# Performance work log

Hardware: AMD Instinct MI355X
Metric: run time of the kernel (lower is better)

Reference implementation:

```python
import math
import jax, jax.numpy as jnp
import numpy as np

T, B, C, H = 1024, 4, 1024, 16
D = C // H  # d_k = 64


def setup_inputs() -> dict:
    key = jax.random.key(0)
    ks = jax.random.split(key, 16)
    s = 0.02
    return {
        "query": jax.random.normal(ks[0], (T, B, C), jnp.float32),
        "key": jax.random.normal(ks[1], (T, B, C), jnp.float32),
        "value": jax.random.normal(ks[2], (T, B, C), jnp.float32),
        "pos_emb": jax.random.normal(ks[3], (2 * T - 1, 1, C), jnp.float32),
        "Wq": jax.random.normal(ks[4], (C, C), jnp.float32) * s,
        "bq": jnp.zeros((C,), jnp.float32),
        "Wk": jax.random.normal(ks[5], (C, C), jnp.float32) * s,
        "bk": jnp.zeros((C,), jnp.float32),
        "Wv": jax.random.normal(ks[6], (C, C), jnp.float32) * s,
        "bv": jnp.zeros((C,), jnp.float32),
        "Wp": jax.random.normal(ks[7], (C, C), jnp.float32) * s,
        "Wo": jax.random.normal(ks[8], (C, C), jnp.float32) * s,
        "bo": jnp.zeros((C,), jnp.float32),
        "pos_bias_u": jax.random.normal(ks[9], (H, D), jnp.float32) * s,
        "pos_bias_v": jax.random.normal(ks[10], (H, D), jnp.float32) * s,
    }


def rel_shift(x):
    # x: [B, H, T, P] with P = 2T-1 -> [B, H, T, T]
    b, h, t, p = x.shape
    x = jnp.pad(x, ((0, 0), (0, 0), (0, 0), (1, 0)))  # [B,H,T,P+1]
    x = x.reshape(b, h, p + 1, t)[:, :, 1:, :].reshape(b, h, t, p)
    return x[..., : p // 2 + 1]


def reference(query, key, value, pos_emb, Wq, bq, Wk, bk, Wv, bv, Wp, Wo, bo,
              pos_bias_u, pos_bias_v):
    # T x B x C -> B x T x C
    q_in = query.transpose(1, 0, 2)
    k_in = key.transpose(1, 0, 2)
    v_in = value.transpose(1, 0, 2)
    p_in = pos_emb.transpose(1, 0, 2)  # [1, 2T-1, C]

    q = (q_in @ Wq.T + bq).reshape(B, T, H, D)            # [B,T,H,D]
    k = (k_in @ Wk.T + bk).reshape(B, T, H, D)
    v = (v_in @ Wv.T + bv).reshape(B, T, H, D)
    p = (p_in @ Wp.T).reshape(2 * T - 1, H, D)            # [2T-1,H,D]

    # content (ac) and position (bd) scores
    matrix_ac = jnp.einsum('bthd,bshd->bhts', q + pos_bias_u, k)   # [B,H,T,T]
    matrix_bd = jnp.einsum('bthd,phd->bhtp', q + pos_bias_v, p)    # [B,H,T,2T-1]
    matrix_bd = rel_shift(matrix_bd)                               # [B,H,T,T]

    scores = (matrix_ac + matrix_bd) / math.sqrt(D)
    scores = jnp.clip(scores, -1e8, 1e8)
    attn = jax.nn.softmax(scores.astype(jnp.float32), axis=-1).astype(scores.dtype)

    x = jnp.einsum('bhts,bshd->bthd', attn, v).reshape(B, T, C)
    out = x @ Wo.T + bo
    return out.transpose(1, 0, 2)  # T x B x C
```

## Files before the change

kernel.cpp:

```cpp
#include <hip/hip_runtime.h>
#include <hip/hip_bf16.h>
#include <math.h>

#define T_SEQ 1024
#define NB 4
#define NH 16
#define DD 64
#define CC 1024

typedef __attribute__((ext_vector_type(8))) short short8;
typedef __attribute__((ext_vector_type(4))) float floatx4;
typedef __attribute__((ext_vector_type(4))) unsigned short ushort4v;

#define MFMA(a, b, c) __builtin_amdgcn_mfma_f32_16x16x32_bf16((a), (b), (c), 0, 0, 0)

__device__ inline float bf2f(unsigned short u) {
  union { unsigned int i; float f; } c; c.i = ((unsigned int)u) << 16; return c.f;
}
__device__ inline unsigned short f2bf(float x) {
  union { float f; unsigned int i; } c; c.f = x;
  unsigned int u = c.i;
  u += 0x7fff + ((u >> 16) & 1);
  return (unsigned short)(u >> 16);
}

__device__ __forceinline__ void gload_lds16(const void* g, void* l) {
  __builtin_amdgcn_global_load_lds(
      (const __attribute__((address_space(1))) unsigned int*)g,
      (__attribute__((address_space(3))) unsigned int*)l, 16, 0, 0);
}

__global__ __launch_bounds__(256) void convert_kernel(
    const float* __restrict__ q, const float* __restrict__ k,
    const float* __restrict__ v, const float* __restrict__ pe_in,
    const float* __restrict__ wq, const float* __restrict__ wk,
    const float* __restrict__ wv, const float* __restrict__ wp,
    const float* __restrict__ wo,
    unsigned short* __restrict__ qo, unsigned short* __restrict__ ko,
    unsigned short* __restrict__ vo, unsigned short* __restrict__ po,
    unsigned short* __restrict__ wqo, unsigned short* __restrict__ wko,
    unsigned short* __restrict__ wvo, unsigned short* __restrict__ wpo,
    unsigned short* __restrict__ woo)
{
  const int i = blockIdx.x * 256 + threadIdx.x;
  const float* src; unsigned short* dst; int off;
  if      (i < 524288)  { src = q;     dst = qo;  off = i; }
  else if (i < 1048576) { src = k;     dst = ko;  off = i - 524288; }
  else if (i < 1572864) { src = v;     dst = vo;  off = i - 1048576; }
  else if (i < 1834880) { src = pe_in; dst = po;  off = i - 1572864; }
  else if (i < 1965952) { src = wq;    dst = wqo; off = i - 1834880; }
  else if (i < 2097024) { src = wk;    dst = wko; off = i - 1965952; }
  else if (i < 2228096) { src = wv;    dst = wvo; off = i - 2097024; }
  else if (i < 2359168) { src = wp;    dst = wpo; off = i - 2228096; }
  else if (i < 2490240) { src = wo;    dst = woo; off = i - 2359168; }
  else {
    const int j = i - 2490240;
    *(short8*)&po[2047 * 1024 + j * 8] = (short8){0, 0, 0, 0, 0, 0, 0, 0};
    return;
  }
  const float4 a0 = *(const float4*)(src + (size_t)off * 8);
  const float4 a1 = *(const float4*)(src + (size_t)off * 8 + 4);
  short8 val = (short8){(short)f2bf(a0.x), (short)f2bf(a0.y), (short)f2bf(a0.z), (short)f2bf(a0.w),
                        (short)f2bf(a1.x), (short)f2bf(a1.y), (short)f2bf(a1.z), (short)f2bf(a1.w)};
  *(short8*)&dst[(size_t)off * 8] = val;
}

template <int OUT_BF16>
__device__ __forceinline__ void gemm_core(
    const unsigned short* __restrict__ A, const unsigned short* __restrict__ Wt,
    const float* __restrict__ bias, void* __restrict__ Cv,
    unsigned short* As, unsigned short* Bs, int N, int K, int bm, int bn)
{
  const int tid = threadIdx.x;
  const int lane = tid & 63;
  const int w = tid >> 6;
  const int l15 = lane & 15, quad = lane >> 4;
  const int rw = (w >> 1) * 64, cw = (w & 1) * 64;

  floatx4 acc[4][4];
#pragma unroll
  for (int i = 0; i < 4; ++i)
#pragma unroll
    for (int j = 0; j < 4; ++j) acc[i][j] = (floatx4){0.f, 0.f, 0.f, 0.f};

  const int lrow = lane >> 2, lcol = (lane & 3) * 8;
  const unsigned short* Ag = A + (size_t)(bm + w * 32 + lrow) * K + lcol;
  const unsigned short* Wg = Wt + (size_t)(bn + w * 32 + lrow) * K + lcol;
  unsigned short* AsW = As + w * 1024;
  unsigned short* BsW = Bs + w * 1024;

  for (int k0 = 0; k0 < K; k0 += 32) {
    gload_lds16(Ag + k0, AsW);
    gload_lds16(Ag + 16 * K + k0, AsW + 512);
    gload_lds16(Wg + k0, BsW);
    gload_lds16(Wg + 16 * K + k0, BsW + 512);
    __syncthreads();

    short8 af[4], bfr[4];
#pragma unroll
    for (int i = 0; i < 4; ++i)
      af[i] = *(short8*)&As[(rw + i * 16 + l15) * 32 + quad * 8];
#pragma unroll
    for (int j = 0; j < 4; ++j)
      bfr[j] = *(short8*)&Bs[(cw + j * 16 + l15) * 32 + quad * 8];
#pragma unroll
    for (int i = 0; i < 4; ++i)
#pragma unroll
      for (int j = 0; j < 4; ++j)
        acc[i][j] = MFMA(af[i], bfr[j], acc[i][j]);
    __syncthreads();
  }

#pragma unroll
  for (int j = 0; j < 4; ++j) {
    const int col = bn + cw + j * 16 + l15;
    const float bj = bias ? bias[col] : 0.f;
#pragma unroll
    for (int i = 0; i < 4; ++i) {
      const int row0 = bm + rw + i * 16 + quad * 4;
#pragma unroll
      for (int reg = 0; reg < 4; ++reg) {
        const float v = acc[i][j][reg] + bj;
        if (OUT_BF16)
          ((unsigned short*)Cv)[(size_t)(row0 + reg) * N + col] = f2bf(v);
        else
          ((float*)Cv)[(size_t)(row0 + reg) * N + col] = v;
      }
    }
  }
}

struct GemmJob { const unsigned short* A; const unsigned short* Wt;
                 const float* bias; unsigned short* C; int mtiles; };
struct GemmJobs { GemmJob j[4]; };

__global__ __launch_bounds__(256) void gemm_qkvp(GemmJobs jobs) {
  __shared__ __align__(16) unsigned short As[128 * 32];
  __shared__ __align__(16) unsigned short Bs[128 * 32];
  GemmJob jb = jobs.j[blockIdx.z];
  if ((int)blockIdx.y >= jb.mtiles) return;
  gemm_core<1>(jb.A, jb.Wt, jb.bias, jb.C, As, Bs, 1024, 1024,
               blockIdx.y * 128, blockIdx.x * 128);
}

template <int OUT_BF16>
__global__ __launch_bounds__(256) void gemm_one(
    const unsigned short* __restrict__ A, const unsigned short* __restrict__ Wt,
    const float* __restrict__ bias, void* __restrict__ Cv) {
  __shared__ __align__(16) unsigned short As[128 * 32];
  __shared__ __align__(16) unsigned short Bs[128 * 32];
  gemm_core<OUT_BF16>(A, Wt, bias, Cv, As, Bs, 1024, 1024,
                      blockIdx.y * 128, blockIdx.x * 128);
}

__global__ __launch_bounds__(256) void transpose_v(
    const unsigned short* __restrict__ vb, unsigned short* __restrict__ vT)
{
  __shared__ __align__(16) unsigned short Lt[64 * 136];
  const int t0 = blockIdx.x * 128;
  const int h = blockIdx.y, b = blockIdx.z;
  const int tid = threadIdx.x;

#pragma unroll
  for (int cc = 0; cc < 4; ++cc) {
    const int idx = tid + cc * 256;
    const int r = idx >> 3, pc = idx & 7;
    short8 val = *(const short8*)(vb + ((size_t)((t0 + r) * 4 + b)) * 1024 + h * 64 + pc * 8);
#pragma unroll
    for (int e = 0; e < 8; ++e)
      Lt[(pc * 8 + e) * 136 + r] = (unsigned short)val[e];
  }
  __syncthreads();
#pragma unroll
  for (int cc = 0; cc < 4; ++cc) {
    const int idx = tid + cc * 256;
    const int d = idx >> 4, tc = idx & 15;
    short8 v2 = *(short8*)&Lt[d * 136 + tc * 8];
    *(short8*)(vT + ((size_t)((b * 16 + h) * 64 + d)) * 1024 + t0 + tc * 8) = v2;
  }
}

__global__ __launch_bounds__(256) void precompute_kernel(
    const unsigned short* __restrict__ kb, const unsigned short* __restrict__ pb,
    const float* __restrict__ pbu, const float* __restrict__ pbv,
    float* __restrict__ uk, float* __restrict__ vp)
{
  const int i = blockIdx.x * 256 + threadIdx.x;
  if (i < 65536) {
    const int b = i >> 14, h = (i >> 10) & 15, s = i & 1023;
    const unsigned short* kr = kb + ((size_t)(s * 4 + b)) * 1024 + h * 64;
    const float* ur = pbu + h * 64;
    float sum = 0.f;
#pragma unroll
    for (int c = 0; c < 8; ++c) {
      short8 kv = *(const short8*)(kr + c * 8);
#pragma unroll
      for (int e = 0; e < 8; ++e) sum += bf2f((unsigned short)kv[e]) * ur[c * 8 + e];
    }
    uk[i] = sum;
  } else if (i < 98304) {
    const int j = i - 65536;
    const int idx = j >> 4, h = j & 15;
    const unsigned short* pr = pb + (size_t)idx * 1024 + h * 64;
    const float* vr = pbv + h * 64;
    float sum = 0.f;
#pragma unroll
    for (int c = 0; c < 8; ++c) {
      short8 pv = *(const short8*)(pr + c * 8);
#pragma unroll
      for (int e = 0; e < 8; ++e) sum += bf2f((unsigned short)pv[e]) * vr[c * 8 + e];
    }
    vp[(idx << 4) + h] = sum;
  }
}

__global__ __launch_bounds__(256) void attn_kernel(
    const unsigned short* __restrict__ qb, const unsigned short* __restrict__ kb,
    const unsigned short* __restrict__ pb, const unsigned short* __restrict__ vT,
    const float* __restrict__ uk, const float* __restrict__ vp,
    unsigned short* __restrict__ xb)
{
  __shared__ __align__(16) unsigned char SU[64 * 196 * 4];
  float* BDf = (float*)SU;
  unsigned short* Pb = (unsigned short*)SU;
  __shared__ float uk_s[128], vp_w[192];
  __shared__ float pmax[2][64], psum[2][64];
  __shared__ float alpha_s[64];

  const int tid = threadIdx.x;
  const int lane = tid & 63;
  const int w = tid >> 6;
  const int l15 = lane & 15, quad = lane >> 4;
  const int th = w & 1, sh = w >> 1;

  const int flat = blockIdx.x + (blockIdx.y << 4) + (blockIdx.z << 8);
  const int x8 = flat & 7, s8 = flat >> 3;
  const int hb = x8 * 8 + (s8 >> 4);
  const int t0 = (s8 & 15) * 64;
  const int b = hb >> 4, h = hb & 15;

  short8 qf[2][2];
#pragma unroll
  for (int tt = 0; tt < 2; ++tt)
#pragma unroll
    for (int kk = 0; kk < 2; ++kk) {
      const int t = t0 + th * 32 + tt * 16 + l15;
      qf[tt][kk] = *(const short8*)(qb + ((size_t)(t * 4 + b)) * 1024 + h * 64 + kk * 32 + quad * 8);
    }

  floatx4 of[2][2];
#pragma unroll
  for (int i = 0; i < 2; ++i)
#pragma unroll
    for (int j = 0; j < 2; ++j) of[i][j] = (floatx4){0.f, 0.f, 0.f, 0.f};

  float m_reg[2] = {-3.0e38f, -3.0e38f};
  float l_reg[2][4] = {{0.f, 0.f, 0.f, 0.f}, {0.f, 0.f, 0.f, 0.f}};

  for (int s0 = 0; s0 < 1024; s0 += 128) {
    const int w0 = s0 - t0 + 960;

    if (tid < 128) uk_s[tid] = uk[((b * 16 + h) << 10) + s0 + tid];
    if (tid < 192) vp_w[tid] = vp[(((size_t)(w0 + tid)) << 4) + h];

#pragma unroll
    for (int jt = 0; jt < 6; ++jt) {
      const int jj = sh * 96 + jt * 16 + l15;
      const unsigned short* pr = pb + ((size_t)(w0 + jj)) * 1024 + h * 64;
      short8 pf0 = *(const short8*)(pr + quad * 8);
      short8 pf1 = *(const short8*)(pr + 32 + quad * 8);
#pragma unroll
      for (int tt = 0; tt < 2; ++tt) {
        floatx4 z = (floatx4){0.f, 0.f, 0.f, 0.f};
        z = MFMA(pf0, qf[tt][0], z);
        z = MFMA(pf1, qf[tt][1], z);
        const int tloc = th * 32 + tt * 16 + l15;
        const int jjb = sh * 96 + jt * 16 + quad * 4;
        *(float4*)&BDf[tloc * 196 + jjb] = make_float4(z[0], z[1], z[2], z[3]);
      }
    }

    floatx4 st[4][2];
#pragma unroll
    for (int stile = 0; stile < 4; ++stile) {
      const int srow = s0 + sh * 64 + stile * 16 + l15;
      const unsigned short* kr = kb + ((size_t)(srow * 4 + b)) * 1024 + h * 64;
      short8 kf0 = *(const short8*)(kr + quad * 8);
      short8 kf1 = *(const short8*)(kr + 32 + quad * 8);
#pragma unroll
      for (int tt = 0; tt < 2; ++tt) {
        floatx4 z = (floatx4){0.f, 0.f, 0.f, 0.f};
        z = MFMA(kf0, qf[tt][0], z);
        z = MFMA(kf1, qf[tt][1], z);
        st[stile][tt] = z;
      }
    }
    __syncthreads();

    float lmax[2] = {-3.0e38f, -3.0e38f};
#pragma unroll
    for (int stile = 0; stile < 4; ++stile)
#pragma unroll
      for (int tt = 0; tt < 2; ++tt) {
        const int tloc = th * 32 + tt * 16 + l15;
#pragma unroll
        for (int reg = 0; reg < 4; ++reg) {
          const int sloc = sh * 64 + stile * 16 + quad * 4 + reg;
          const int jj = sloc - tloc + 63;
          float v = 0.125f * (st[stile][tt][reg] + BDf[tloc * 196 + jj] +
                              uk_s[sloc] + vp_w[jj]);
          st[stile][tt][reg] = v;
          lmax[tt] = fmaxf(lmax[tt], v);
        }
      }
#pragma unroll
    for (int tt = 0; tt < 2; ++tt) {
      lmax[tt] = fmaxf(lmax[tt], __shfl_xor(lmax[tt], 16));
      lmax[tt] = fmaxf(lmax[tt], __shfl_xor(lmax[tt], 32));
    }
    if (quad == 0) {
      pmax[sh][th * 32 + l15] = lmax[0];
      pmax[sh][th * 32 + 16 + l15] = lmax[1];
    }
    __syncthreads();

    float alpha_sc[2];
#pragma unroll
    for (int tt = 0; tt < 2; ++tt) {
      const int t = th * 32 + tt * 16 + l15;
      const float mn = fmaxf(m_reg[tt], fmaxf(pmax[0][t], pmax[1][t]));
      alpha_sc[tt] = __expf(m_reg[tt] - mn);
      m_reg[tt] = mn;
    }
    if (sh == 0 && quad == 0) {
      alpha_s[th * 32 + l15] = alpha_sc[0];
      alpha_s[th * 32 + 16 + l15] = alpha_sc[1];
    }
    float lsum[2] = {0.f, 0.f};
#pragma unroll
    for (int stile = 0; stile < 4; ++stile)
#pragma unroll
      for (int tt = 0; tt < 2; ++tt) {
        float p0 = __expf(st[stile][tt][0] - m_reg[tt]);
        float p1 = __expf(st[stile][tt][1] - m_reg[tt]);
        float p2 = __expf(st[stile][tt][2] - m_reg[tt]);
        float p3 = __expf(st[stile][tt][3] - m_reg[tt]);
        lsum[tt] += p0 + p1 + p2 + p3;
        const int tloc = th * 32 + tt * 16 + l15;
        const int sb = sh * 64 + stile * 16 + quad * 4;
        ushort4v pk = (ushort4v){f2bf(p0), f2bf(p1), f2bf(p2), f2bf(p3)};
        *(ushort4v*)&Pb[tloc * 136 + sb] = pk;
      }
#pragma unroll
    for (int tt = 0; tt < 2; ++tt) {
      lsum[tt] += __shfl_xor(lsum[tt], 16);
      lsum[tt] += __shfl_xor(lsum[tt], 32);
    }
    if (quad == 0) {
      psum[sh][th * 32 + l15] = lsum[0];
      psum[sh][th * 32 + 16 + l15] = lsum[1];
    }
    __syncthreads();

#pragma unroll
    for (int tt = 0; tt < 2; ++tt)
#pragma unroll
      for (int reg = 0; reg < 4; ++reg) {
        const int t = th * 32 + tt * 16 + quad * 4 + reg;
        const float ar = alpha_s[t];
        of[tt][0][reg] *= ar;
        of[tt][1][reg] *= ar;
        l_reg[tt][reg] = l_reg[tt][reg] * ar + psum[0][t] + psum[1][t];
      }
#pragma unroll
    for (int kk2 = 0; kk2 < 4; ++kk2) {
      short8 pa[2], vf[2];
#pragma unroll
      for (int tt = 0; tt < 2; ++tt)
        pa[tt] = *(short8*)&Pb[(th * 32 + tt * 16 + l15) * 136 + kk2 * 32 + quad * 8];
#pragma unroll
      for (int dt = 0; dt < 2; ++dt)
        vf[dt] = *(const short8*)(vT + ((size_t)((b * 16 + h) * 64 + sh * 32 + dt * 16 + l15)) * 1024 +
                                  s0 + kk2 * 32 + quad * 8);
#pragma unroll
      for (int tt = 0; tt < 2; ++tt)
#pragma unroll
        for (int dt = 0; dt < 2; ++dt)
          of[tt][dt] = MFMA(pa[tt], vf[kk2 * 0 + dt], of[tt][dt]);
    }
    __syncthreads();
  }

#pragma unroll
  for (int tt = 0; tt < 2; ++tt)
#pragma unroll
    for (int reg = 0; reg < 4; ++reg) {
      const int t = th * 32 + tt * 16 + quad * 4 + reg;
      const float il = 1.f / l_reg[tt][reg];
#pragma unroll
      for (int dt = 0; dt < 2; ++dt) {
        const int d = sh * 32 + dt * 16 + l15;
        xb[((size_t)((t0 + t) * 4 + b)) * 1024 + h * 64 + d] = f2bf(of[tt][dt][reg] * il);
      }
    }
}

extern "C" void kernel_launch(void* const* d_in, const int* in_sizes, int n_in,
                              void* d_out, int out_size, void* d_ws, size_t ws_size,
                              hipStream_t stream) {
  const float* query   = (const float*)d_in[0];
  const float* key_    = (const float*)d_in[1];
  const float* value   = (const float*)d_in[2];
  const float* pos_emb = (const float*)d_in[3];
  const float* Wq  = (const float*)d_in[4];
  const float* bq  = (const float*)d_in[5];
  const float* Wk  = (const float*)d_in[6];
  const float* bk  = (const float*)d_in[7];
  const float* Wv  = (const float*)d_in[8];
  const float* bv  = (const float*)d_in[9];
  const float* Wp  = (const float*)d_in[10];
  const float* Wo  = (const float*)d_in[11];
  const float* bo  = (const float*)d_in[12];
  const float* pbu = (const float*)d_in[13];
  const float* pbv = (const float*)d_in[14];
  float* out = (float*)d_out;

  unsigned short* U = (unsigned short*)d_ws;
  unsigned short* qin = U;
  unsigned short* kin = U + 4194304;
  unsigned short* vin = U + 8388608;
  unsigned short* pe  = U + 12582912;
  unsigned short* wq  = U + 14680064;
  unsigned short* wk  = U + 15728640;
  unsigned short* wv  = U + 16777216;
  unsigned short* wp  = U + 17825792;
  unsigned short* wo  = U + 18874368;
  unsigned short* qb  = U + 19922944;
  unsigned short* kb  = U + 24117248;
  unsigned short* pb  = U + 28311552;
  unsigned short* vpo = U + 30408704;
  unsigned short* vTb = pe;
  unsigned short* xb  = qin;
  float* fbase = (float*)(U + 34603008);
  float* uk = fbase;
  float* vp = fbase + 65536;

  const dim3 blk(256);

  convert_kernel<<<dim3(9728), blk, 0, stream>>>(
      query, key_, value, pos_emb, Wq, Wk, Wv, Wp, Wo,
      qin, kin, vin, pe, wq, wk, wv, wp, wo);

  GemmJobs jobs;
  jobs.j[0] = GemmJob{qin, wq, bq, qb, 32};
  jobs.j[1] = GemmJob{kin, wk, bk, kb, 32};
  jobs.j[2] = GemmJob{vin, wv, bv, vpo, 32};
  jobs.j[3] = GemmJob{pe,  wp, nullptr, pb, 16};
  gemm_qkvp<<<dim3(8, 32, 4), blk, 0, stream>>>(jobs);

  transpose_v<<<dim3(8, 16, 4), blk, 0, stream>>>(vpo, vTb);

  precompute_kernel<<<dim3(384), blk, 0, stream>>>(kb, pb, pbu, pbv, uk, vp);

  attn_kernel<<<dim3(16, 16, 4), blk, 0, stream>>>(qb, kb, pb, vTb, uk, vp, xb);

  gemm_one<0><<<dim3(8, 32), blk, 0, stream>>>(xb, wo, bo, out);
}
```

Before: 364.5 us.

## Give each wave its own 16 query rows to drop block-wide softmax syncs

The attention kernel is restructured so each of the four waves owns 16 query rows and processes the full 128-key tile, instead of splitting the tile across waves in a 2x2 grid. Softmax max and sum reductions become in-wave shuffles, and the per-wave BD and P buffers live in private shared-memory slices, so the per-iteration __syncthreads barriers are removed. The uk and vp bias vectors are loaded once per block into shared memory, and vp is folded into BD when it is written. In exchange, each wave computes a wider position band (10 tiles vs 6 per pair) and loads K and V redundantly, which adds global/L2 traffic and MFMA work per block.

```diff
diff --git a/kernel.cpp b/kernel.cpp
--- a/kernel.cpp
+++ b/kernel.cpp
@@ -220,18 +220,15 @@
     const float* __restrict__ uk, const float* __restrict__ vp,
     unsigned short* __restrict__ xb)
 {
-  __shared__ __align__(16) unsigned char SU[64 * 196 * 4];
-  float* BDf = (float*)SU;
-  unsigned short* Pb = (unsigned short*)SU;
-  __shared__ float uk_s[128], vp_w[192];
-  __shared__ float pmax[2][64], psum[2][64];
-  __shared__ float alpha_s[64];
+  __shared__ __align__(16) float BDs[4][16][164];
+  __shared__ __align__(16) unsigned short Pw[4][16][136];
+  __shared__ __align__(16) float uk_full[1024];
+  __shared__ __align__(16) float vp_full[1104];
 
   const int tid = threadIdx.x;
   const int lane = tid & 63;
   const int w = tid >> 6;
   const int l15 = lane & 15, quad = lane >> 4;
-  const int th = w & 1, sh = w >> 1;
 
   const int flat = blockIdx.x + (blockIdx.y << 4) + (blockIdx.z << 8);
   const int x8 = flat & 7, s8 = flat >> 3;
@@ -239,170 +236,123 @@
   const int t0 = (s8 & 15) * 64;
   const int b = hb >> 4, h = hb & 15;
 
-  short8 qf[2][2];
-#pragma unroll
-  for (int tt = 0; tt < 2; ++tt)
-#pragma unroll
-    for (int kk = 0; kk < 2; ++kk) {
-      const int t = t0 + th * 32 + tt * 16 + l15;
-      qf[tt][kk] = *(const short8*)(qb + ((size_t)(t * 4 + b)) * 1024 + h * 64 + kk * 32 + quad * 8);
-    }
-
-  floatx4 of[2][2];
-#pragma unroll
-  for (int i = 0; i < 2; ++i)
-#pragma unroll
-    for (int j = 0; j < 2; ++j) of[i][j] = (floatx4){0.f, 0.f, 0.f, 0.f};
-
-  float m_reg[2] = {-3.0e38f, -3.0e38f};
-  float l_reg[2][4] = {{0.f, 0.f, 0.f, 0.f}, {0.f, 0.f, 0.f, 0.f}};
+  for (int i = tid; i < 1024; i += 256) uk_full[i] = uk[((b * 16 + h) << 10) + i];
+  const int gbase = 960 - t0;
+  for (int i = tid; i < 1104; i += 256) {
+    int g = gbase + i; g = g > 2047 ? 2047 : g;
+    vp_full[i] = vp[(g << 4) + h];
+  }
+  __syncthreads();
+
+  const int tw = t0 + w * 16;
+
+  short8 qf[2];
+#pragma unroll
+  for (int kk = 0; kk < 2; ++kk)
+    qf[kk] = *(const short8*)(qb + ((size_t)((tw + l15) * 4 + b)) * 1024 + h * 64 + kk * 32 + quad * 8);
+
+  floatx4 of[4];
+#pragma unroll
+  for (int dt = 0; dt < 4; ++dt) of[dt] = (floatx4){0.f, 0.f, 0.f, 0.f};
+  float m_ln = -3.0e38f, l_ln = 0.f;
+
+  float* BDw = &BDs[w][0][0];
+  unsigned short* Pww = &Pw[w][0][0];
+  const unsigned short* vTh = vT + ((size_t)((b * 16 + h) * 64)) * 1024;
 
   for (int s0 = 0; s0 < 1024; s0 += 128) {
-    const int w0 = s0 - t0 + 960;
-
-    if (tid < 128) uk_s[tid] = uk[((b * 16 + h) << 10) + s0 + tid];
-    if (tid < 192) vp_w[tid] = vp[(((size_t)(w0 + tid)) << 4) + h];
-
-#pragma unroll
-    for (int jt = 0; jt < 6; ++jt) {
-      const int jj = sh * 96 + jt * 16 + l15;
-      const unsigned short* pr = pb + ((size_t)(w0 + jj)) * 1024 + h * 64;
+    const int pbase = s0 - t0 + 1008 - w * 16;
+    const int vbase = s0 - w * 16 + 48;
+
+#pragma unroll
+    for (int jt = 0; jt < 10; ++jt) {
+      const unsigned short* pr = pb + (size_t)(pbase + jt * 16 + l15) * 1024 + h * 64;
       short8 pf0 = *(const short8*)(pr + quad * 8);
       short8 pf1 = *(const short8*)(pr + 32 + quad * 8);
-#pragma unroll
-      for (int tt = 0; tt < 2; ++tt) {
-        floatx4 z = (floatx4){0.f, 0.f, 0.f, 0.f};
-        z = MFMA(pf0, qf[tt][0], z);
-        z = MFMA(pf1, qf[tt][1], z);
-        const int tloc = th * 32 + tt * 16 + l15;
-        const int jjb = sh * 96 + jt * 16 + quad * 4;
-        *(float4*)&BDf[tloc * 196 + jjb] = make_float4(z[0], z[1], z[2], z[3]);
-      }
-    }
-
-    floatx4 st[4][2];
-#pragma unroll
-    for (int stile = 0; stile < 4; ++stile) {
-      const int srow = s0 + sh * 64 + stile * 16 + l15;
+      floatx4 z = (floatx4){0.f, 0.f, 0.f, 0.f};
+      z = MFMA(pf0, qf[0], z);
+      z = MFMA(pf1, qf[1], z);
+      const float4 vpv = *(const float4*)&vp_full[vbase + jt * 16 + quad * 4];
+      float4 o;
+      o.x = z[0] + vpv.x; o.y = z[1] + vpv.y; o.z = z[2] + vpv.z; o.w = z[3] + vpv.w;
+      *(float4*)&BDw[l15 * 164 + jt * 16 + quad * 4] = o;
+    }
+
+    floatx4 st[8];
+#pragma unroll
+    for (int stile = 0; stile < 8; ++stile) {
+      const int srow = s0 + stile * 16 + l15;
       const unsigned short* kr = kb + ((size_t)(srow * 4 + b)) * 1024 + h * 64;
       short8 kf0 = *(const short8*)(kr + quad * 8);
       short8 kf1 = *(const short8*)(kr + 32 + quad * 8);
-#pragma unroll
-      for (int tt = 0; tt < 2; ++tt) {
-        floatx4 z = (floatx4){0.f, 0.f, 0.f, 0.f};
-        z = MFMA(kf0, qf[tt][0], z);
-        z = MFMA(kf1, qf[tt][1], z);
-        st[stile][tt] = z;
+      floatx4 z = (floatx4){0.f, 0.f, 0.f, 0.f};
+      z = MFMA(kf0, qf[0], z);
+      z = MFMA(kf1, qf[1], z);
+      st[stile] = z;
+    }
+
+    float lmax = -3.0e38f;
+#pragma unroll
+    for (int stile = 0; stile < 8; ++stile) {
+      const float4 uk4 = *(const float4*)&uk_full[s0 + stile * 16 + quad * 4];
+      const int jb = stile * 16 + quad * 4 - l15 + 15;
+#pragma unroll
+      for (int reg = 0; reg < 4; ++reg) {
+        const float ukr = reg == 0 ? uk4.x : (reg == 1 ? uk4.y : (reg == 2 ? uk4.z : uk4.w));
+        float v = 0.125f * (st[stile][reg] + BDw[l15 * 164 + jb + reg] + ukr);
+        st[stile][reg] = v;
+        lmax = fmaxf(lmax, v);
       }
     }
-    __syncthreads();
-
-    float lmax[2] = {-3.0e38f, -3.0e38f};
-#pragma unroll
-    for (int stile = 0; stile < 4; ++stile)
-#pragma unroll
-      for (int tt = 0; tt < 2; ++tt) {
-        const int tloc = th * 32 + tt * 16 + l15;
-#pragma unroll
-        for (int reg = 0; reg < 4; ++reg) {
-          const int sloc = sh * 64 + stile * 16 + quad * 4 + reg;
-          const int jj = sloc - tloc + 63;
-          float v = 0.125f * (st[stile][tt][reg] + BDf[tloc * 196 + jj] +
-                              uk_s[sloc] + vp_w[jj]);
-          st[stile][tt][reg] = v;
-          lmax[tt] = fmaxf(lmax[tt], v);
-        }
+    lmax = fmaxf(lmax, __shfl_xor(lmax, 16));
+    lmax = fmaxf(lmax, __shfl_xor(lmax, 32));
+    const float mn = fmaxf(m_ln, lmax);
+    const float alpha = __expf(m_ln - mn);
+    m_ln = mn;
+
+    float lsum = 0.f;
+#pragma unroll
+    for (int stile = 0; stile < 8; ++stile) {
+      float p0 = __expf(st[stile][0] - mn);
+      float p1 = __expf(st[stile][1] - mn);
+      float p2 = __expf(st[stile][2] - mn);
+      float p3 = __expf(st[stile][3] - mn);
+      lsum += p0 + p1 + p2 + p3;
+      ushort4v pk = (ushort4v){f2bf(p0), f2bf(p1), f2bf(p2), f2bf(p3)};
+      *(ushort4v*)&Pww[l15 * 136 + stile * 16 + quad * 4] = pk;
+    }
+    lsum += __shfl_xor(lsum, 16);
+    lsum += __shfl_xor(lsum, 32);
+    l_ln = l_ln * alpha + lsum;
+
+#pragma unroll
+    for (int reg = 0; reg < 4; ++reg) {
+      const float ar = __shfl(alpha, quad * 4 + reg);
+#pragma unroll
+      for (int dt = 0; dt < 4; ++dt) of[dt][reg] *= ar;
+    }
+#pragma unroll
+    for (int kk = 0; kk < 4; ++kk) {
+      const short8 pa = *(short8*)&Pww[l15 * 136 + kk * 32 + quad * 8];
+#pragma unroll
+      for (int dt = 0; dt < 4; ++dt) {
+        const short8 vf = *(const short8*)(vTh + (size_t)(dt * 16 + l15) * 1024 + s0 + kk * 32 + quad * 8);
+        of[dt] = MFMA(pa, vf, of[dt]);
       }
-#pragma unroll
-    for (int tt = 0; tt < 2; ++tt) {
-      lmax[tt] = fmaxf(lmax[tt], __shfl_xor(lmax[tt], 16));
-      lmax[tt] = fmaxf(lmax[tt], __shfl_xor(lmax[tt], 32));
-    }
-    if (quad == 0) {
-      pmax[sh][th * 32 + l15] = lmax[0];
-      pmax[sh][th * 32 + 16 + l15] = lmax[1];
-    }
-    __syncthreads();
-
-    float alpha_sc[2];
-#pragma unroll
-    for (int tt = 0; tt < 2; ++tt) {
-      const int t = th * 32 + tt * 16 + l15;
-      const float mn = fmaxf(m_reg[tt], fmaxf(pmax[0][t], pmax[1][t]));
-      alpha_sc[tt] = __expf(m_reg[tt] - mn);
-      m_reg[tt] = mn;
-    }
-    if (sh == 0 && quad == 0) {
-      alpha_s[th * 32 + l15] = alpha_sc[0];
-      alpha_s[th * 32 + 16 + l15] = alpha_sc[1];
-    }
-    float lsum[2] = {0.f, 0.f};
-#pragma unroll
-    for (int stile = 0; stile < 4; ++stile)
-#pragma unroll
-      for (int tt = 0; tt < 2; ++tt) {
-        float p0 = __expf(st[stile][tt][0] - m_reg[tt]);
-        float p1 = __expf(st[stile][tt][1] - m_reg[tt]);
-        float p2 = __expf(st[stile][tt][2] - m_reg[tt]);
-        float p3 = __expf(st[stile][tt][3] - m_reg[tt]);
-        lsum[tt] += p0 + p1 + p2 + p3;
-        const int tloc = th * 32 + tt * 16 + l15;
-        const int sb = sh * 64 + stile * 16 + quad * 4;
-        ushort4v pk = (ushort4v){f2bf(p0), f2bf(p1), f2bf(p2), f2bf(p3)};
-        *(ushort4v*)&Pb[tloc * 136 + sb] = pk;
-      }
-#pragma unroll
-    for (int tt = 0; tt < 2; ++tt) {
-      lsum[tt] += __shfl_xor(lsum[tt], 16);
-      lsum[tt] += __shfl_xor(lsum[tt], 32);
-    }
-    if (quad == 0) {
-      psum[sh][th * 32 + l15] = lsum[0];
-      psum[sh][th * 32 + 16 + l15] = lsum[1];
-    }
-    __syncthreads();
-
-#pragma unroll
-    for (int tt = 0; tt < 2; ++tt)
-#pragma unroll
-      for (int reg = 0; reg < 4; ++reg) {
-        const int t = th * 32 + tt * 16 + quad * 4 + reg;
-        const float ar = alpha_s[t];
-        of[tt][0][reg] *= ar;
-        of[tt][1][reg] *= ar;
-        l_reg[tt][reg] = l_reg[tt][reg] * ar + psum[0][t] + psum[1][t];
-      }
-#pragma unroll
-    for (int kk2 = 0; kk2 < 4; ++kk2) {
-      short8 pa[2], vf[2];
-#pragma unroll
-      for (int tt = 0; tt < 2; ++tt)
-        pa[tt] = *(short8*)&Pb[(th * 32 + tt * 16 + l15) * 136 + kk2 * 32 + quad * 8];
-#pragma unroll
-      for (int dt = 0; dt < 2; ++dt)
-        vf[dt] = *(const short8*)(vT + ((size_t)((b * 16 + h) * 64 + sh * 32 + dt * 16 + l15)) * 1024 +
-                                  s0 + kk2 * 32 + quad * 8);
-#pragma unroll
-      for (int tt = 0; tt < 2; ++tt)
-#pragma unroll
-        for (int dt = 0; dt < 2; ++dt)
-          of[tt][dt] = MFMA(pa[tt], vf[kk2 * 0 + dt], of[tt][dt]);
-    }
-    __syncthreads();
-  }
-
-#pragma unroll
-  for (int tt = 0; tt < 2; ++tt)
-#pragma unroll
-    for (int reg = 0; reg < 4; ++reg) {
-      const int t = th * 32 + tt * 16 + quad * 4 + reg;
-      const float il = 1.f / l_reg[tt][reg];
-#pragma unroll
-      for (int dt = 0; dt < 2; ++dt) {
-        const int d = sh * 32 + dt * 16 + l15;
-        xb[((size_t)((t0 + t) * 4 + b)) * 1024 + h * 64 + d] = f2bf(of[tt][dt][reg] * il);
-      }
-    }
+    }
+  }
+
+#pragma unroll
+  for (int reg = 0; reg < 4; ++reg) {
+    const float lr = __shfl(l_ln, quad * 4 + reg);
+    const float il = 1.f / lr;
+    const int t = tw + quad * 4 + reg;
+#pragma unroll
+    for (int dt = 0; dt < 4; ++dt) {
+      const int d = dt * 16 + l15;
+      xb[((size_t)(t * 4 + b)) * 1024 + h * 64 + d] = f2bf(of[dt][reg] * il);
+    }
+  }
 }
 
 extern "C" void kernel_launch(void* const* d_in, const int* in_sizes, int n_in,
```

New measurement: 438.2 us. 20.2% more time.
